# Kernel optimization log

Hardware: AMD Instinct MI355X
Metric: run time of the kernel (lower is better)

Reference implementation:

```python
import jax, jax.numpy as jnp
import numpy as np

# OPT-1.3b-like attention dims
B, S, E, NH, HD = 1, 2048, 2048, 32, 64
Q_BITS, R_BITS, BASE_GS, R_GS = 1, 3, 16, 16


def quotrem_fake_quantize(x, q_bits=Q_BITS, r_bits=R_BITS, base_gs=BASE_GS, r_gs=R_GS):
    r_max = 2 ** (r_bits - 1) - 1
    r_min = -r_max - 1
    eps = 1e-8
    shape = x.shape
    H = shape[-1]
    xg = x.reshape(shape[:-1] + (H // base_gs, base_gs))  # [..., G_base, base_gs]
    max_abs = jnp.maximum(jnp.max(jnp.abs(xg), axis=-1, keepdims=True), eps)
    if q_bits == 1:
        log2_max = jnp.log2(max_abs)
        base_floor = jnp.exp2(jnp.floor(log2_max))
        base_ceil = jnp.exp2(jnp.ceil(log2_max))
        base = jnp.where(jnp.abs(max_abs - base_floor) <= jnp.abs(base_ceil - max_abs),
                         base_floor, base_ceil)
        base = jnp.clip(base, 1.0, 128.0)
        max_pos = jnp.max(xg, axis=-1, keepdims=True)
        min_val = jnp.min(xg, axis=-1, keepdims=True)
        sign_flag = jnp.where(jnp.abs(max_pos) >= jnp.abs(min_val), 1.0, -1.0)
        q = (xg * sign_flag >= base / 2.0).astype(x.dtype)
        q_scaled = q * sign_flag * base
    else:
        q_max = 2 ** (q_bits - 1) - 1
        threshold = max_abs / q_max
        base = jnp.full_like(threshold, 64.0)
        for b in (32.0, 16.0, 8.0, 4.0, 2.0):
            base = jnp.where(threshold <= b, jnp.full_like(threshold, b), base)
        q = jnp.clip(jnp.round(xg / base), -q_max, q_max)
        q_scaled = q * base
    r = (xg - q_scaled).reshape(shape)
    rg = r.reshape(shape[:-1] + (H // r_gs, r_gs))  # [..., G_r, r_gs]
    max_abs_r = jnp.maximum(jnp.max(jnp.abs(rg), axis=-1, keepdims=True), eps)
    scale_r = max_abs_r / r_max
    r_q = jnp.clip(jnp.round(rg / scale_r), r_min, r_max)
    r_dq = (r_q * scale_r).reshape(shape)
    return q_scaled.reshape(shape) + r_dq


def setup_inputs() -> dict:
    key = jax.random.key(0)
    ks = jax.random.split(key, 9)
    w = lambda k: jax.random.normal(k, (E, E), dtype=jnp.float32) * 0.02
    b = lambda k: jax.random.normal(k, (E,), dtype=jnp.float32) * 0.02
    return {
        "hidden_states": jax.random.normal(ks[0], (B, S, E), dtype=jnp.float32),
        "Wq": w(ks[1]), "bq": b(ks[2]),
        "Wk": w(ks[3]), "bk": b(ks[4]),
        "Wv": w(ks[5]), "bv": b(ks[6]),
        "Wo": w(ks[7]), "bo": b(ks[8]),
    }


def reference(hidden_states, Wq, bq, Wk, bk, Wv, bv, Wo, bo):
    scaling = HD ** -0.5
    heads = lambda x: x.reshape(B, S, NH, HD).transpose(0, 2, 1, 3)  # [B,NH,S,HD]
    q = heads((hidden_states @ Wq.T + bq) * scaling)
    k = quotrem_fake_quantize(heads(hidden_states @ Wk.T + bk))
    v = quotrem_fake_quantize(heads(hidden_states @ Wv.T + bv))
    scores = jnp.einsum('bhqd,bhkd->bhqk', q, k)
    idx = jnp.arange(S)
    scores = jnp.where(idx[:, None] >= idx[None, :], scores, -jnp.inf)  # causal
    attn = jax.nn.softmax(scores, axis=-1)
    out = jnp.einsum('bhqk,bhkd->bhqd', attn, v).transpose(0, 2, 1, 3).reshape(B, S, E)
    return out @ Wo.T + bo
```

## Files before the change

### kernel.cpp

```cpp
#include <hip/hip_runtime.h>
#include <math.h>

#define SEQ 2048
#define EMB 2048
#define NHEAD 32
#define HDIM 64

typedef unsigned short u16;
typedef _Float16 half8 __attribute__((ext_vector_type(8)));
typedef _Float16 half4 __attribute__((ext_vector_type(4)));
typedef __attribute__((ext_vector_type(4))) float floatx4;

__device__ __forceinline__ floatx4 mfma_f16(half8 a, half8 b, floatx4 c) {
    return __builtin_amdgcn_mfma_f32_16x16x32_f16(a, b, c, 0, 0, 0);
}
__device__ __forceinline__ void load16(const u16* g, u16* l) {
    __builtin_amdgcn_global_load_lds(
        (const __attribute__((address_space(1))) unsigned int*)g,
        (__attribute__((address_space(3))) unsigned int*)l, 16, 0, 0);
}
__device__ __forceinline__ u16 h2u(_Float16 h) { return *reinterpret_cast<u16*>(&h); }

__global__ __launch_bounds__(256)
void cvt5(const float* __restrict__ X0, u16* __restrict__ Y0,
          const float* __restrict__ X1, u16* __restrict__ Y1,
          const float* __restrict__ X2, u16* __restrict__ Y2,
          const float* __restrict__ X3, u16* __restrict__ Y3,
          const float* __restrict__ X4, u16* __restrict__ Y4)
{
    const float* Xs[5] = {X0, X1, X2, X3, X4};
    u16* Ys[5] = {Y0, Y1, Y2, Y3, Y4};
    const float* X = Xs[blockIdx.y];
    u16* Y = Ys[blockIdx.y];
    const int i = (blockIdx.x * 256 + threadIdx.x) * 4;
    float4 v = *reinterpret_cast<const float4*>(X + i);
    half4 hv;
    hv.x = (_Float16)v.x; hv.y = (_Float16)v.y;
    hv.z = (_Float16)v.z; hv.w = (_Float16)v.w;
    *reinterpret_cast<half4*>(Y + i) = hv;
}

template<int MODE>
__global__ __launch_bounds__(256)
void gemm16(const u16* __restrict__ A,
            const u16* __restrict__ B0, const u16* __restrict__ B1,
            const u16* __restrict__ B2,
            const float* __restrict__ bk, const float* __restrict__ bv,
            const float* __restrict__ bq,
            float* __restrict__ F0, float* __restrict__ F1a,
            float* __restrict__ F1b, u16* __restrict__ Qb)
{
    __shared__ __align__(16) u16 As[128 * 64];
    __shared__ __align__(16) u16 Bs[128 * 64];

    const int tid = threadIdx.x;
    const int w = tid >> 6, lane = tid & 63;
    const int quad = lane >> 4, colk = lane & 15;
    const int bn = blockIdx.x, bm = blockIdx.y, z = blockIdx.z;
    const int wm = (w & 1) * 64, wn = (w >> 1) * 64;
    const int k0 = (MODE == 1) ? z * 1024 : 0;
    const int nk = (MODE == 1) ? 1024 : 2048;

    const u16* Bg = (MODE == 1) ? B0 : ((z == 0) ? B0 : (z == 1) ? B1 : B2);

    const int srow = tid >> 3, sphy = tid & 7;
    const int sLog = (sphy - srow) & 7;
    size_t agof[4], bgof[4];
    int ldst[4];
    #pragma unroll
    for (int p = 0; p < 4; ++p) {
        const int row = srow + 32 * p;
        agof[p] = (size_t)(bm * 128 + row) * EMB + k0 + sLog * 8;
        bgof[p] = (size_t)(bn * 128 + row) * EMB + k0 + sLog * 8;
        ldst[p] = (tid + 256 * p) * 8;
    }

    const int aoct0 = ((quad + colk) & 7) * 8;
    const int aoct1 = ((quad + 4 + colk) & 7) * 8;

    floatx4 acc[4][4];
    #pragma unroll
    for (int i = 0; i < 4; ++i)
        #pragma unroll
        for (int j = 0; j < 4; ++j) acc[i][j] = (floatx4){0.f, 0.f, 0.f, 0.f};

    for (int kt = 0; kt < nk; kt += 64) {
        __syncthreads();
        #pragma unroll
        for (int p = 0; p < 4; ++p) {
            load16(A  + agof[p] + kt, As + ldst[p]);
            load16(Bg + bgof[p] + kt, Bs + ldst[p]);
        }
        __syncthreads();

        half8 a0[4], a1[4], b0[4], b1[4];
        #pragma unroll
        for (int i = 0; i < 4; ++i) {
            a0[i] = *reinterpret_cast<const half8*>(&As[(wm + 16*i + colk) * 64 + aoct0]);
            a1[i] = *reinterpret_cast<const half8*>(&As[(wm + 16*i + colk) * 64 + aoct1]);
        }
        #pragma unroll
        for (int j = 0; j < 4; ++j) {
            b0[j] = *reinterpret_cast<const half8*>(&Bs[(wn + 16*j + colk) * 64 + aoct0]);
            b1[j] = *reinterpret_cast<const half8*>(&Bs[(wn + 16*j + colk) * 64 + aoct1]);
        }
        #pragma unroll
        for (int i = 0; i < 4; ++i)
            #pragma unroll
            for (int j = 0; j < 4; ++j) {
                acc[i][j] = mfma_f16(a0[i], b0[j], acc[i][j]);
                acc[i][j] = mfma_f16(a1[i], b1[j], acc[i][j]);
            }
    }

    const float* bias = (z == 0) ? bk : (z == 1) ? bv : bq;
    #pragma unroll
    for (int i = 0; i < 4; ++i) {
        const int row = bm * 128 + wm + 16*i + 4*quad;
        #pragma unroll
        for (int j = 0; j < 4; ++j) {
            const int col = bn * 128 + wn + 16*j + colk;
            const float bv2 = (MODE == 0) ? bias[col] : 0.f;
            #pragma unroll
            for (int r = 0; r < 4; ++r) {
                const size_t idx = (size_t)(row + r) * EMB + col;
                if (MODE == 1) {
                    float* Fo = (z == 0) ? F0 : ((bm < 8) ? F1a : F1b - 2097152);
                    Fo[idx] = acc[i][j][r];
                } else if (z == 2) {
                    ((_Float16*)Qb)[idx] = (_Float16)((acc[i][j][r] + bv2) * 0.125f);
                } else {
                    float* Fo = z ? F1a : F0;
                    Fo[idx] = acc[i][j][r] + bv2;
                }
            }
        }
    }
}

__global__ __launch_bounds__(256)
void add_bias(const float* __restrict__ P0, const float* __restrict__ P1a,
              const float* __restrict__ P1b, const float* __restrict__ bias,
              float* __restrict__ out)
{
    const int i = (blockIdx.x * 256 + threadIdx.x) * 4;
    const float* P1 = (i < 2097152) ? P1a + i : P1b + (i - 2097152);
    const float4 a = *reinterpret_cast<const float4*>(P0 + i);
    const float4 b = *reinterpret_cast<const float4*>(P1);
    const float4 c = *reinterpret_cast<const float4*>(bias + (i & (EMB - 1)));
    float4 o;
    o.x = a.x + b.x + c.x; o.y = a.y + b.y + c.y;
    o.z = a.z + b.z + c.z; o.w = a.w + b.w + c.w;
    *reinterpret_cast<float4*>(out + i) = o;
}

__device__ __forceinline__ void quotrem16(float* x)
{
    float maxabs = 1e-8f, maxpos = -INFINITY, minval = INFINITY;
    #pragma unroll
    for (int i = 0; i < 16; ++i) {
        maxabs = fmaxf(maxabs, fabsf(x[i]));
        maxpos = fmaxf(maxpos, x[i]);
        minval = fminf(minval, x[i]);
    }
    const float lg = log2f(maxabs);
    const float bfl = exp2f(floorf(lg));
    const float bcl = exp2f(ceilf(lg));
    float base = (fabsf(maxabs - bfl) <= fabsf(bcl - maxabs)) ? bfl : bcl;
    base = fminf(fmaxf(base, 1.0f), 128.0f);
    const float sgn = (fabsf(maxpos) >= fabsf(minval)) ? 1.0f : -1.0f;
    const float hb = 0.5f * base, sb = sgn * base;

    float qs[16], r[16], maxr = 1e-8f;
    #pragma unroll
    for (int i = 0; i < 16; ++i) {
        qs[i] = (x[i] * sgn >= hb) ? sb : 0.0f;
        r[i]  = x[i] - qs[i];
        maxr  = fmaxf(maxr, fabsf(r[i]));
    }
    const float scale = maxr / 3.0f;
    #pragma unroll
    for (int i = 0; i < 16; ++i) {
        float rq = rintf(r[i] / scale);
        rq = fminf(fmaxf(rq, -4.0f), 3.0f);
        x[i] = qs[i] + rq * scale;
    }
}

__global__ __launch_bounds__(256)
void quant_kv(const float* __restrict__ FK, u16* __restrict__ Kb,
              const float* __restrict__ FV, u16* __restrict__ Vt)
{
    __shared__ u16 T[64 * 264];
    const int bid = blockIdx.x, t = threadIdx.x;

    if (bid < 1024) {
        const int g = bid * 256 + t;
        const float* p = FK + (size_t)g * 16;
        float x[16];
        #pragma unroll
        for (int i = 0; i < 16; i += 4)
            *reinterpret_cast<float4*>(&x[i]) = *reinterpret_cast<const float4*>(p + i);
        quotrem16(x);
        _Float16* o = (_Float16*)Kb + (size_t)g * 16;
        #pragma unroll
        for (int i = 0; i < 16; ++i) o[i] = (_Float16)x[i];
        return;
    }

    const int l = bid - 1024;
    const int sb = l >> 5, h = l & 31;
    const float* src = FV + (size_t)(sb * 256 + t) * EMB + h * HDIM;

    #pragma unroll
    for (int g4 = 0; g4 < 4; ++g4) {
        float x[16];
        #pragma unroll
        for (int i = 0; i < 16; i += 4)
            *reinterpret_cast<float4*>(&x[i]) =
                *reinterpret_cast<const float4*>(src + g4 * 16 + i);
        quotrem16(x);
        #pragma unroll
        for (int i = 0; i < 16; ++i)
            T[(g4 * 16 + i) * 264 + t] = h2u((_Float16)x[i]);
    }
    __syncthreads();

    const int d = t >> 2, seg = t & 3;
    u16* dst = Vt + (size_t)(h * HDIM + d) * SEQ + sb * 256 + seg * 64;
    #pragma unroll
    for (int jj = 0; jj < 8; ++jj)
        *reinterpret_cast<half8*>(dst + jj * 8) =
            *reinterpret_cast<const half8*>(&T[d * 264 + seg * 64 + jj * 8]);
}

__global__ __launch_bounds__(256)
void flash128(const u16* __restrict__ Qb, const u16* __restrict__ Kb,
              const u16* __restrict__ Vt, u16* __restrict__ Ob)
{
    __shared__ __align__(16) u16 Ks[128 * 64];
    __shared__ __align__(16) u16 Vs[64 * 128];
    __shared__ __align__(16) u16 Ps[64 * 136];

    const int tid = threadIdx.x;
    const int w = tid >> 6, lane = tid & 63;
    const int quad = lane >> 4, colk = lane & 15;
    const int pairb = blockIdx.x;
    const int h = blockIdx.y;

    int krow[4], koff[4], vd[4], voff[4];
    #pragma unroll
    for (int p = 0; p < 4; ++p) {
        const int c = tid + p * 256;
        krow[p] = c >> 3;
        koff[p] = (((c & 7) - krow[p]) & 7) * 8;
        vd[p]   = c >> 4;
        voff[p] = (((c & 15) - vd[p]) & 15) * 8;
    }
    const int ldb0 = w * 512;
    const int kp0 = ((quad + colk) & 7) * 8;
    const int kp1 = ((quad + 4 + colk) & 7) * 8;

    #pragma unroll
    for (int pass = 0; pass < 2; ++pass) {
        const int qt = pass ? (31 - pairb) : pairb;
        const int nw = (qt + 2) >> 1;
        const int qrow_g = qt * 64 + 16 * w + colk;

        __syncthreads();
        #pragma unroll
        for (int p = 0; p < 2; ++p) {
            const int c = tid + p * 256, row = c >> 3, cq = c & 7;
            *reinterpret_cast<half8*>(&Ps[row * 136 + cq * 8]) =
                *reinterpret_cast<const half8*>(&Qb[(size_t)(qt * 64 + row) * EMB + h * HDIM + cq * 8]);
        }
        __syncthreads();
        const half8 qb0 = *reinterpret_cast<const half8*>(&Ps[(16*w + colk) * 136 + quad * 8]);
        const half8 qb1 = *reinterpret_cast<const half8*>(&Ps[(16*w + colk) * 136 + 32 + quad * 8]);

        floatx4 o[4];
        #pragma unroll
        for (int t = 0; t < 4; ++t) o[t] = (floatx4){0.f, 0.f, 0.f, 0.f};
        float lsum = 0.f;

        for (int kw = 0; kw < nw; ++kw) {
            __syncthreads();
            #pragma unroll
            for (int p = 0; p < 4; ++p) {
                load16(Kb + (size_t)(kw * 128 + krow[p]) * EMB + h * HDIM + koff[p],
                       Ks + p * 2048 + ldb0);
                load16(Vt + (size_t)(h * HDIM + vd[p]) * SEQ + kw * 128 + voff[p],
                       Vs + p * 2048 + ldb0);
            }
            __syncthreads();

            floatx4 s[8];
            #pragma unroll
            for (int t = 0; t < 8; ++t) {
                const half8 kb0 = *reinterpret_cast<const half8*>(&Ks[(16*t + colk) * 64 + kp0]);
                const half8 kb1 = *reinterpret_cast<const half8*>(&Ks[(16*t + colk) * 64 + kp1]);
                floatx4 zz = (floatx4){0.f, 0.f, 0.f, 0.f};
                zz = mfma_f16(kb0, qb0, zz);
                s[t] = mfma_f16(kb1, qb1, zz);
            }
            if (kw == nw - 1) {
                #pragma unroll
                for (int t = 0; t < 8; ++t)
                    #pragma unroll
                    for (int r = 0; r < 4; ++r)
                        if (kw * 128 + 16*t + 4*quad + r > qrow_g) s[t][r] = -INFINITY;
            }

            #pragma unroll
            for (int t = 0; t < 8; ++t) {
                half4 pw;
                float pv0 = __expf(s[t][0] - 4.0f), pv1 = __expf(s[t][1] - 4.0f);
                float pv2 = __expf(s[t][2] - 4.0f), pv3 = __expf(s[t][3] - 4.0f);
                lsum += (pv0 + pv1) + (pv2 + pv3);
                pw.x = (_Float16)pv0; pw.y = (_Float16)pv1;
                pw.z = (_Float16)pv2; pw.w = (_Float16)pv3;
                *reinterpret_cast<half4*>(&Ps[(16*w + colk) * 136 + 16*t + 4*quad]) = pw;
            }

            half8 pa[4];
            #pragma unroll
            for (int seg = 0; seg < 4; ++seg)
                pa[seg] = *reinterpret_cast<const half8*>(&Ps[(16*w + colk) * 136 + seg * 32 + quad * 8]);
            #pragma unroll
            for (int t = 0; t < 4; ++t) {
                #pragma unroll
                for (int seg = 0; seg < 4; ++seg) {
                    const int vp = ((4*seg + quad + colk) & 15) * 8;
                    const half8 vb = *reinterpret_cast<const half8*>(&Vs[(16*t + colk) * 128 + vp]);
                    o[t] = mfma_f16(pa[seg], vb, o[t]);
                }
            }
        }

        lsum += __shfl_xor(lsum, 16, 64);
        lsum += __shfl_xor(lsum, 32, 64);

        float invr[4];
        #pragma unroll
        for (int r = 0; r < 4; ++r) invr[r] = 1.0f / __shfl(lsum, 4*quad + r, 64);
        #pragma unroll
        for (int t = 0; t < 4; ++t)
            #pragma unroll
            for (int r = 0; r < 4; ++r) {
                const int row = qt * 64 + 16*w + 4*quad + r;
                ((_Float16*)Ob)[(size_t)row * EMB + h * HDIM + 16*t + colk] =
                    (_Float16)(o[t][r] * invr[r]);
            }
    }
}

extern "C" void kernel_launch(void* const* d_in, const int* in_sizes, int n_in,
                              void* d_out, int out_size, void* d_ws, size_t ws_size,
                              hipStream_t stream)
{
    const float* hidden = (const float*)d_in[0];
    const float* Wq = (const float*)d_in[1];
    const float* bq = (const float*)d_in[2];
    const float* Wk = (const float*)d_in[3];
    const float* bk = (const float*)d_in[4];
    const float* Wv = (const float*)d_in[5];
    const float* bv = (const float*)d_in[6];
    const float* Wo = (const float*)d_in[7];
    const float* bo = (const float*)d_in[8];
    float* out = (float*)d_out;

    char* ws = (char*)d_ws;
    const size_t MB = 1024 * 1024;
    u16*   H16  = (u16*)(ws);
    u16*   Wk16 = (u16*)(ws + 8 * MB);
    u16*   Wv16 = (u16*)(ws + 16 * MB);
    float* FK   = (float*)(ws + 24 * MB);
    float* FV   = (float*)(ws + 40 * MB);
    u16*   Qbuf = (u16*)(ws + 56 * MB);
    u16*   Kbuf = (u16*)(ws + 8 * MB);
    u16*   Vtb  = (u16*)(ws + 16 * MB);
    u16*   Obuf = (u16*)(ws);
    float* FO1a = (float*)(ws + 32 * MB);
    float* FO0  = (float*)(ws + 40 * MB);
    float* FO1b = (float*)(ws + 56 * MB);
    u16*   Wq16 = (u16*)d_out;
    u16*   Wo16 = (u16*)((char*)d_out + 8 * MB);

    const dim3 cb(256);
    float* nilf = nullptr; u16* nil16 = nullptr;

    hipLaunchKernelGGL(cvt5, dim3(4096, 5), cb, 0, stream,
                       hidden, H16, Wk, Wk16, Wv, Wv16, Wq, Wq16, Wo, Wo16);
    hipLaunchKernelGGL((gemm16<0>), dim3(16, 16, 3), cb, 0, stream,
                       H16, Wk16, Wv16, Wq16, bk, bv, bq, FK, FV, nilf, Qbuf);
    hipLaunchKernelGGL(quant_kv, dim3(1280), cb, 0, stream, FK, Kbuf, FV, Vtb);
    hipLaunchKernelGGL(flash128, dim3(16, NHEAD), cb, 0, stream,
                       Qbuf, Kbuf, Vtb, Obuf);
    hipLaunchKernelGGL((gemm16<1>), dim3(16, 16, 2), cb, 0, stream,
                       Obuf, Wo16, nil16, nil16, nilf, nilf, nilf,
                       FO0, FO1a, FO1b, nil16);
    hipLaunchKernelGGL(add_bias, dim3(4096), cb, 0, stream,
                       FO0, FO1a, FO1b, bo, out);
}
```

Before: 306.7 us.

## Drop split-K output GEMM and bias kernel, fuse Wo conversion into quant kernel

The output projection no longer splits K into two halves written to partial fp32 buffers and summed by a separate add_bias kernel. It now runs as a single full-K GEMM that adds the bias and writes straight to the output. The Wo fp32-to-fp16 conversion moves from the initial conversion kernel into extra blocks of the quant_kv kernel, and workspace buffers are reassigned to fit. This removes one launch and the partial-sum memory traffic, but the output GEMM now has only 256 blocks, which may underfill the GPU.

```diff
diff --git a/kernel.cpp b/kernel.cpp
--- a/kernel.cpp
+++ b/kernel.cpp
@@ -22,14 +22,13 @@
 __device__ __forceinline__ u16 h2u(_Float16 h) { return *reinterpret_cast<u16*>(&h); }
 
 __global__ __launch_bounds__(256)
-void cvt5(const float* __restrict__ X0, u16* __restrict__ Y0,
+void cvt4(const float* __restrict__ X0, u16* __restrict__ Y0,
           const float* __restrict__ X1, u16* __restrict__ Y1,
           const float* __restrict__ X2, u16* __restrict__ Y2,
-          const float* __restrict__ X3, u16* __restrict__ Y3,
-          const float* __restrict__ X4, u16* __restrict__ Y4)
-{
-    const float* Xs[5] = {X0, X1, X2, X3, X4};
-    u16* Ys[5] = {Y0, Y1, Y2, Y3, Y4};
+          const float* __restrict__ X3, u16* __restrict__ Y3)
+{
+    const float* Xs[4] = {X0, X1, X2, X3};
+    u16* Ys[4] = {Y0, Y1, Y2, Y3};
     const float* X = Xs[blockIdx.y];
     u16* Y = Ys[blockIdx.y];
     const int i = (blockIdx.x * 256 + threadIdx.x) * 4;
@@ -40,15 +39,14 @@
     *reinterpret_cast<half4*>(Y + i) = hv;
 }
 
-template<int MODE>
 __global__ __launch_bounds__(256)
 void gemm16(const u16* __restrict__ A,
             const u16* __restrict__ B0, const u16* __restrict__ B1,
             const u16* __restrict__ B2,
             const float* __restrict__ bk, const float* __restrict__ bv,
             const float* __restrict__ bq,
-            float* __restrict__ F0, float* __restrict__ F1a,
-            float* __restrict__ F1b, u16* __restrict__ Qb)
+            float* __restrict__ F0, float* __restrict__ F1,
+            u16* __restrict__ Qb)
 {
     __shared__ __align__(16) u16 As[128 * 64];
     __shared__ __align__(16) u16 Bs[128 * 64];
@@ -58,10 +56,8 @@
     const int quad = lane >> 4, colk = lane & 15;
     const int bn = blockIdx.x, bm = blockIdx.y, z = blockIdx.z;
     const int wm = (w & 1) * 64, wn = (w >> 1) * 64;
-    const int k0 = (MODE == 1) ? z * 1024 : 0;
-    const int nk = (MODE == 1) ? 1024 : 2048;
-
-    const u16* Bg = (MODE == 1) ? B0 : ((z == 0) ? B0 : (z == 1) ? B1 : B2);
+
+    const u16* Bg = (z == 0) ? B0 : (z == 1) ? B1 : B2;
 
     const int srow = tid >> 3, sphy = tid & 7;
     const int sLog = (sphy - srow) & 7;
@@ -70,8 +66,8 @@
     #pragma unroll
     for (int p = 0; p < 4; ++p) {
         const int row = srow + 32 * p;
-        agof[p] = (size_t)(bm * 128 + row) * EMB + k0 + sLog * 8;
-        bgof[p] = (size_t)(bn * 128 + row) * EMB + k0 + sLog * 8;
+        agof[p] = (size_t)(bm * 128 + row) * EMB + sLog * 8;
+        bgof[p] = (size_t)(bn * 128 + row) * EMB + sLog * 8;
         ldst[p] = (tid + 256 * p) * 8;
     }
 
@@ -84,7 +80,7 @@
         #pragma unroll
         for (int j = 0; j < 4; ++j) acc[i][j] = (floatx4){0.f, 0.f, 0.f, 0.f};
 
-    for (int kt = 0; kt < nk; kt += 64) {
+    for (int kt = 0; kt < 2048; kt += 64) {
         __syncthreads();
         #pragma unroll
         for (int p = 0; p < 4; ++p) {
@@ -120,38 +116,17 @@
         #pragma unroll
         for (int j = 0; j < 4; ++j) {
             const int col = bn * 128 + wn + 16*j + colk;
-            const float bv2 = (MODE == 0) ? bias[col] : 0.f;
+            const float bv2 = bias[col];
             #pragma unroll
             for (int r = 0; r < 4; ++r) {
                 const size_t idx = (size_t)(row + r) * EMB + col;
-                if (MODE == 1) {
-                    float* Fo = (z == 0) ? F0 : ((bm < 8) ? F1a : F1b - 2097152);
-                    Fo[idx] = acc[i][j][r];
-                } else if (z == 2) {
+                if (z == 2)
                     ((_Float16*)Qb)[idx] = (_Float16)((acc[i][j][r] + bv2) * 0.125f);
-                } else {
-                    float* Fo = z ? F1a : F0;
-                    Fo[idx] = acc[i][j][r] + bv2;
-                }
-            }
-        }
-    }
-}
-
-__global__ __launch_bounds__(256)
-void add_bias(const float* __restrict__ P0, const float* __restrict__ P1a,
-              const float* __restrict__ P1b, const float* __restrict__ bias,
-              float* __restrict__ out)
-{
-    const int i = (blockIdx.x * 256 + threadIdx.x) * 4;
-    const float* P1 = (i < 2097152) ? P1a + i : P1b + (i - 2097152);
-    const float4 a = *reinterpret_cast<const float4*>(P0 + i);
-    const float4 b = *reinterpret_cast<const float4*>(P1);
-    const float4 c = *reinterpret_cast<const float4*>(bias + (i & (EMB - 1)));
-    float4 o;
-    o.x = a.x + b.x + c.x; o.y = a.y + b.y + c.y;
-    o.z = a.z + b.z + c.z; o.w = a.w + b.w + c.w;
-    *reinterpret_cast<float4*>(out + i) = o;
+                else
+                    ((z == 0) ? F0 : F1)[idx] = acc[i][j][r] + bv2;
+            }
+        }
+    }
 }
 
 __device__ __forceinline__ void quotrem16(float* x)
@@ -189,10 +164,21 @@
 
 __global__ __launch_bounds__(256)
 void quant_kv(const float* __restrict__ FK, u16* __restrict__ Kb,
-              const float* __restrict__ FV, u16* __restrict__ Vt)
+              const float* __restrict__ FV, u16* __restrict__ Vt,
+              const float* __restrict__ Wo, u16* __restrict__ Wo16)
 {
     __shared__ u16 T[64 * 264];
     const int bid = blockIdx.x, t = threadIdx.x;
+
+    if (bid >= 1280) {
+        const int i = ((bid - 1280) * 256 + t) * 4;
+        float4 v = *reinterpret_cast<const float4*>(Wo + i);
+        half4 hv;
+        hv.x = (_Float16)v.x; hv.y = (_Float16)v.y;
+        hv.z = (_Float16)v.z; hv.w = (_Float16)v.w;
+        *reinterpret_cast<half4*>(Wo16 + i) = hv;
+        return;
+    }
 
     if (bid < 1024) {
         const int g = bid * 256 + t;
@@ -379,26 +365,22 @@
     u16*   Qbuf = (u16*)(ws + 56 * MB);
     u16*   Kbuf = (u16*)(ws + 8 * MB);
     u16*   Vtb  = (u16*)(ws + 16 * MB);
-    u16*   Obuf = (u16*)(ws);
-    float* FO1a = (float*)(ws + 32 * MB);
-    float* FO0  = (float*)(ws + 40 * MB);
-    float* FO1b = (float*)(ws + 56 * MB);
+    u16*   Wo16 = (u16*)(ws);
+    u16*   Obuf = (u16*)(ws + 24 * MB);
     u16*   Wq16 = (u16*)d_out;
-    u16*   Wo16 = (u16*)((char*)d_out + 8 * MB);
 
     const dim3 cb(256);
     float* nilf = nullptr; u16* nil16 = nullptr;
 
-    hipLaunchKernelGGL(cvt5, dim3(4096, 5), cb, 0, stream,
-                       hidden, H16, Wk, Wk16, Wv, Wv16, Wq, Wq16, Wo, Wo16);
-    hipLaunchKernelGGL((gemm16<0>), dim3(16, 16, 3), cb, 0, stream,
-                       H16, Wk16, Wv16, Wq16, bk, bv, bq, FK, FV, nilf, Qbuf);
-    hipLaunchKernelGGL(quant_kv, dim3(1280), cb, 0, stream, FK, Kbuf, FV, Vtb);
+    hipLaunchKernelGGL(cvt4, dim3(4096, 4), cb, 0, stream,
+                       hidden, H16, Wk, Wk16, Wv, Wv16, Wq, Wq16);
+    hipLaunchKernelGGL(gemm16, dim3(16, 16, 3), cb, 0, stream,
+                       H16, Wk16, Wv16, Wq16, bk, bv, bq, FK, FV, Qbuf);
+    hipLaunchKernelGGL(quant_kv, dim3(1280 + 4096), cb, 0, stream,
+                       FK, Kbuf, FV, Vtb, Wo, Wo16);
     hipLaunchKernelGGL(flash128, dim3(16, NHEAD), cb, 0, stream,
                        Qbuf, Kbuf, Vtb, Obuf);
-    hipLaunchKernelGGL((gemm16<1>), dim3(16, 16, 2), cb, 0, stream,
-                       Obuf, Wo16, nil16, nil16, nilf, nilf, nilf,
-                       FO0, FO1a, FO1b, nil16);
-    hipLaunchKernelGGL(add_bias, dim3(4096), cb, 0, stream,
-                       FO0, FO1a, FO1b, bo, out);
-}
+    hipLaunchKernelGGL(gemm16, dim3(16, 16, 1), cb, 0, stream,
+                       Obuf, Wo16, nil16, nil16, bo, nilf, nilf,
+                       out, nilf, nil16);
+}
```

Result: no change. 308.0 us (+0.4%).
